# Kernel tuning notes

Measured on AMD Instinct MI355X. Metric: run time of the kernel, lower is better.

Reference implementation:

```python
import jax, jax.numpy as jnp
import numpy as np

N_USERS = 100000
N_MOVIES = 20000
E = 1000000
D_USER = 128
D_MOVIE = 404
HID = 256
OUT = 128


def setup_inputs() -> dict:
    key = jax.random.key(0)
    ks = jax.random.split(key, 20)
    s = 0.05
    inp = {
        'x_user': jax.random.normal(ks[0], (N_USERS, D_USER), jnp.float32),
        'x_movie': jax.random.normal(ks[1], (N_MOVIES, D_MOVIE), jnp.float32),
        'edge_src': jax.random.randint(ks[2], (E,), 0, N_USERS, jnp.int32),
        'edge_dst': jax.random.randint(ks[3], (E,), 0, N_MOVIES, jnp.int32),
        # layer 1, relation user-rates->movie: lin_l (on aggregated user msgs, with bias), lin_r (root, no bias)
        'w1_rm_l': jax.random.normal(ks[4], (D_USER, HID), jnp.float32) * s,
        'b1_rm': jnp.zeros((HID,), jnp.float32),
        'w1_rm_r': jax.random.normal(ks[5], (D_MOVIE, HID), jnp.float32) * s,
        # layer 1, relation movie-rev_rates->user
        'w1_mu_l': jax.random.normal(ks[6], (D_MOVIE, HID), jnp.float32) * s,
        'b1_mu': jnp.zeros((HID,), jnp.float32),
        'w1_mu_r': jax.random.normal(ks[7], (D_USER, HID), jnp.float32) * s,
        # layer 2, relation user-rates->movie
        'w2_rm_l': jax.random.normal(ks[8], (HID, OUT), jnp.float32) * s,
        'b2_rm': jnp.zeros((OUT,), jnp.float32),
        'w2_rm_r': jax.random.normal(ks[9], (HID, OUT), jnp.float32) * s,
        # layer 2, relation movie-rev_rates->user
        'w2_mu_l': jax.random.normal(ks[10], (HID, OUT), jnp.float32) * s,
        'b2_mu': jnp.zeros((OUT,), jnp.float32),
        'w2_mu_r': jax.random.normal(ks[11], (HID, OUT), jnp.float32) * s,
    }
    return inp


def _seg_mean(msgs, dst, n_dst):
    # mean-aggregate edge messages [E, d] into destination nodes [n_dst, d]
    s = jax.ops.segment_sum(msgs, dst, num_segments=n_dst)
    cnt = jax.ops.segment_sum(jnp.ones((dst.shape[0], 1), msgs.dtype), dst, num_segments=n_dst)
    return s / jnp.maximum(cnt, 1.0)


def _sage(x_src, x_dst, src, dst, n_dst, w_l, b_l, w_r):
    # PyG SAGEConv (mean aggr): lin_l(mean_{j->i} x_j) + lin_r(x_i)
    agg = _seg_mean(x_src[src], dst, n_dst)
    return agg @ w_l + b_l + x_dst @ w_r


def reference(x_user, x_movie, edge_src, edge_dst,
              w1_rm_l, b1_rm, w1_rm_r, w1_mu_l, b1_mu, w1_mu_r,
              w2_rm_l, b2_rm, w2_rm_r, w2_mu_l, b2_mu, w2_mu_r):
    # layer 1 (HeteroConv sum aggr is trivial: one relation per dst type) + relu
    h_movie = jax.nn.relu(_sage(x_user, x_movie, edge_src, edge_dst, N_MOVIES, w1_rm_l, b1_rm, w1_rm_r))
    h_user = jax.nn.relu(_sage(x_movie, x_user, edge_dst, edge_src, N_USERS, w1_mu_l, b1_mu, w1_mu_r))
    # layer 2 (no relu, matching the torch module)
    out_movie = _sage(h_user, h_movie, edge_src, edge_dst, N_MOVIES, w2_rm_l, b2_rm, w2_rm_r)
    out_user = _sage(h_movie, h_user, edge_dst, edge_src, N_USERS, w2_mu_l, b2_mu, w2_mu_r)
    return (out_movie, out_user)
```

## Files before the change

kernel.cpp:

```cpp
#include <hip/hip_runtime.h>
#include <cstddef>
#include <cstdint>

#define E_EDGES 1000000
#define NU 100000
#define NM 20000
#define DU 128
#define DM 404
#define HIDDIM 256
#define OUTDIM 128
#define XMW 544

typedef short bf8_t __attribute__((ext_vector_type(8)));
typedef float f32x4 __attribute__((ext_vector_type(4)));
typedef unsigned short u16x8 __attribute__((ext_vector_type(8)));

__device__ __forceinline__ float b2f(unsigned short u) {
  union { unsigned int i; float f; } x; x.i = ((unsigned int)u) << 16; return x.f;
}
__device__ __forceinline__ unsigned short f2b(float f) {
  union { float f; unsigned int i; } x; x.f = f;
  unsigned int r = x.i + 0x7FFFu + ((x.i >> 16) & 1u);
  return (unsigned short)(r >> 16);
}

#define GLOAD_LDS16(gp, lp)                                                      \
  __builtin_amdgcn_global_load_lds(                                              \
      (const __attribute__((address_space(1))) unsigned int*)(gp),               \
      (__attribute__((address_space(3))) unsigned int*)(lp), 16, 0, 0)

#define HISTB 977
__global__ __launch_bounds__(256) void hist_kernel(
    const int* __restrict__ esrc, const int* __restrict__ edst,
    int* __restrict__ deg_u, int* __restrict__ deg_m,
    int* __restrict__ rank_u, int* __restrict__ rank_m) {
  int e4 = blockIdx.x * 256 + threadIdx.x;
  if (e4 >= E_EDGES / 4) return;
  int4 s4 = reinterpret_cast<const int4*>(esrc)[e4];
  int4 d4 = reinterpret_cast<const int4*>(edst)[e4];
  int4 ru, rm;
  ru.x = atomicAdd(&deg_u[s4.x], 1);
  ru.y = atomicAdd(&deg_u[s4.y], 1);
  ru.z = atomicAdd(&deg_u[s4.z], 1);
  ru.w = atomicAdd(&deg_u[s4.w], 1);
  rm.x = atomicAdd(&deg_m[d4.x], 1);
  rm.y = atomicAdd(&deg_m[d4.y], 1);
  rm.z = atomicAdd(&deg_m[d4.z], 1);
  rm.w = atomicAdd(&deg_m[d4.w], 1);
  reinterpret_cast<int4*>(rank_u)[e4] = ru;
  reinterpret_cast<int4*>(rank_m)[e4] = rm;
}

__device__ __forceinline__ void scan_core_256(const int* __restrict__ deg,
                                              int* __restrict__ off, int n,
                                              int* wsum) {
  const int tid = threadIdx.x;
  const int lane = tid & 63;
  const int w = tid >> 6;
  int carry = 0;
  for (int base = 0; base < n; base += 4096) {
    const int i0 = base + tid * 16;
    int v[16];
    int s = 0;
    if (i0 + 16 <= n) {
#pragma unroll
      for (int q = 0; q < 4; ++q) {
        int4 t4 = *reinterpret_cast<const int4*>(&deg[i0 + q * 4]);
        v[q * 4 + 0] = t4.x; v[q * 4 + 1] = t4.y; v[q * 4 + 2] = t4.z; v[q * 4 + 3] = t4.w;
      }
    } else {
#pragma unroll
      for (int j = 0; j < 16; ++j) v[j] = (i0 + j < n) ? deg[i0 + j] : 0;
    }
#pragma unroll
    for (int j = 0; j < 16; ++j) s += v[j];
    int ws_ = s;
#pragma unroll
    for (int d = 1; d < 64; d <<= 1) {
      int t = __shfl_up(ws_, d, 64);
      if (lane >= d) ws_ += t;
    }
    if (lane == 63) wsum[w] = ws_;
    __syncthreads();
    int woff = 0, ctot = 0;
#pragma unroll
    for (int j = 0; j < 4; ++j) {
      int x = wsum[j];
      if (j < w) woff += x;
      ctot += x;
    }
    int ex = carry + woff + ws_ - s;
    if (i0 + 16 <= n) {
      int o[16];
#pragma unroll
      for (int j = 0; j < 16; ++j) { o[j] = ex; ex += v[j]; }
#pragma unroll
      for (int q = 0; q < 4; ++q)
        *reinterpret_cast<int4*>(&off[i0 + q * 4]) =
            make_int4(o[q * 4], o[q * 4 + 1], o[q * 4 + 2], o[q * 4 + 3]);
    } else {
#pragma unroll
      for (int j = 0; j < 16; ++j) {
        if (i0 + j < n) off[i0 + j] = ex;
        ex += v[j];
      }
    }
    carry += ctot;
    __syncthreads();
  }
  if (tid == 0) off[n] = carry;
}

#define PRA 3200000
#define PRB 5280000
#define PRC 5722368
__global__ __launch_bounds__(256) void scanprep_kernel(
    const int* __restrict__ deg_m, int* __restrict__ off_m,
    const int* __restrict__ deg_u, int* __restrict__ off_u,
    const float* __restrict__ x_user, unsigned short* __restrict__ xu_bf,
    const float* __restrict__ x_movie, unsigned short* __restrict__ xmcat,
    const float* __restrict__ w1_rm_l, const float* __restrict__ w1_rm_r,
    const float* __restrict__ w1_mu_l, const float* __restrict__ w1_mu_r,
    const float* __restrict__ w2_rm_l, const float* __restrict__ w2_mu_r,
    const float* __restrict__ w2_mu_l, const float* __restrict__ w2_rm_r,
    unsigned short* __restrict__ wL1, unsigned short* __restrict__ w1mur,
    unsigned short* __restrict__ wL2u, unsigned short* __restrict__ w2mul,
    unsigned short* __restrict__ w2rmr) {
  __shared__ int wsum[4];
  if (blockIdx.x == 0) { scan_core_256(deg_m, off_m, NM, wsum); return; }
  if (blockIdx.x == 1) { scan_core_256(deg_u, off_u, NU, wsum); return; }
  int j = (blockIdx.x - 2) * 256 + threadIdx.x;
  if (j < PRA) {
    float4 v = reinterpret_cast<const float4*>(x_user)[j];
    ushort4 o;
    o.x = f2b(v.x); o.y = f2b(v.y); o.z = f2b(v.z); o.w = f2b(v.w);
    reinterpret_cast<ushort4*>(xu_bf)[j] = o;
  } else if (j < PRB) {
    int q = j - PRA;
    int row = q / 104, c4 = (q % 104) * 4;
    ushort4 o;
    if (c4 < DM) {
      float4 v = *reinterpret_cast<const float4*>(&x_movie[(size_t)row * DM + c4]);
      o.x = f2b(v.x); o.y = f2b(v.y); o.z = f2b(v.z); o.w = f2b(v.w);
    } else {
      o.x = o.y = o.z = o.w = 0;
    }
    *reinterpret_cast<ushort4*>(&xmcat[(size_t)row * XMW + 128 + c4]) = o;
  } else if (j < PRC) {
    int q = j - PRB;
    if (q < 278528) {
      int n = q / 544, k = q % 544;
      float v = 0.f;
      if (n < 256) {
        if (k < 128) v = w1_rm_l[(size_t)k * 256 + n];
        else if (k < 532) v = w1_rm_r[(size_t)(k - 128) * 256 + n];
      } else {
        if (k >= 128 && k < 532) v = w1_mu_l[(size_t)(k - 128) * 256 + (n - 256)];
      }
      wL1[q] = f2b(v);
    } else if (q < 311296) {
      int p = q - 278528; int n = p / 128, k = p % 128;
      w1mur[p] = f2b(w1_mu_r[(size_t)k * 256 + n]);
    } else if (q < 376832) {
      int p = q - 311296; int n = p / 256, k = p % 256;
      float v = (n < 128) ? w2_rm_l[(size_t)k * 128 + n] : w2_mu_r[(size_t)k * 128 + (n - 128)];
      wL2u[p] = f2b(v);
    } else if (q < 409600) {
      int p = q - 376832; int n = p / 256, k = p % 256;
      w2mul[p] = f2b(w2_mu_l[(size_t)k * 128 + n]);
    } else {
      int p = q - 409600; int n = p / 256, k = p % 256;
      w2rmr[p] = f2b(w2_rm_r[(size_t)k * 128 + n]);
    }
  }
}

template <int MODE>
__device__ __forceinline__ void gemm_core(
    const unsigned short* __restrict__ A, int lda,
    const unsigned short* __restrict__ Bt, int ldb, int K,
    const unsigned short* __restrict__ elem, const float* __restrict__ bias,
    void* __restrict__ outA, int M, int bx, int by,
    unsigned short* Alds, unsigned short* Blds) {
  const int tid = threadIdx.x;
  const int w = tid >> 6, l = tid & 63;
  const int row0 = bx * 128;
  const int col0 = by * 128;
  const int wr = w >> 1, wc = w & 1;

  f32x4 acc[4][4] = {};

  int ar0 = row0 + w * 32 + (l >> 2);
  int ar1 = ar0 + 16;
  if (ar0 >= M) ar0 = M - 1;
  if (ar1 >= M) ar1 = M - 1;
  const size_t aoff0 = (size_t)ar0 * lda + (l & 3) * 8;
  const size_t aoff1 = (size_t)ar1 * lda + (l & 3) * 8;
  const int nr0 = col0 + w * 32 + (l >> 2);
  const size_t boff0 = (size_t)nr0 * ldb + (l & 3) * 8;
  const size_t boff1 = (size_t)(nr0 + 16) * ldb + (l & 3) * 8;
  unsigned short* aldsb = &Alds[w * 1024];
  unsigned short* bldsb = &Blds[w * 1024];

  for (int k0 = 0; k0 < K; k0 += 32) {
    GLOAD_LDS16(A + aoff0 + k0, aldsb);
    GLOAD_LDS16(A + aoff1 + k0, aldsb + 512);
    GLOAD_LDS16(Bt + boff0 + k0, bldsb);
    GLOAD_LDS16(Bt + boff1 + k0, bldsb + 512);
    __syncthreads();
    bf8_t af[4], bfr[4];
#pragma unroll
    for (int mi = 0; mi < 4; ++mi)
      af[mi] = *reinterpret_cast<const bf8_t*>(&Alds[(wr * 64 + mi * 16 + (l & 15)) * 32 + (l >> 4) * 8]);
#pragma unroll
    for (int nj = 0; nj < 4; ++nj)
      bfr[nj] = *reinterpret_cast<const bf8_t*>(&Blds[(wc * 64 + nj * 16 + (l & 15)) * 32 + (l >> 4) * 8]);
#pragma unroll
    for (int mi = 0; mi < 4; ++mi)
#pragma unroll
      for (int nj = 0; nj < 4; ++nj)
        acc[mi][nj] = __builtin_amdgcn_mfma_f32_16x16x32_bf16(af[mi], bfr[nj], acc[mi][nj], 0, 0, 0);
    __syncthreads();
  }

#pragma unroll
  for (int mi = 0; mi < 4; ++mi) {
    const int rbase = row0 + wr * 64 + mi * 16 + ((l >> 4) << 2);
#pragma unroll
    for (int nj = 0; nj < 4; ++nj) {
      const int col = col0 + wc * 64 + nj * 16 + (l & 15);
      float bb = 0.0f;
      if constexpr (MODE == 0 || MODE == 1 || MODE == 6) bb = bias[col];
#pragma unroll
      for (int r = 0; r < 4; ++r) {
        const int row = rbase + r;
        if (row >= M) continue;
        float v = acc[mi][nj][r] + bb;
        if constexpr (MODE == 1) v += b2f(elem[(size_t)row * 256 + col]);
        if constexpr (MODE == 0 || MODE == 1) v = fmaxf(v, 0.0f);
        if constexpr (MODE == 0 || MODE == 1 || MODE == 5) {
          ((unsigned short*)outA)[(size_t)row * 256 + col] = f2b(v);
        } else if constexpr (MODE == 2) {
          ((unsigned short*)outA)[(size_t)row * 128 + col] = f2b(v);
        } else {
          ((float*)outA)[(size_t)row * 128 + col] = v;
        }
      }
    }
  }
}

#define FILLB 977
__global__ __launch_bounds__(256) void fill_t1_kernel(
    const int* __restrict__ esrc, const int* __restrict__ edst,
    const int* __restrict__ rank_m, const int* __restrict__ rank_u,
    const int* __restrict__ off_m, const int* __restrict__ off_u,
    int* __restrict__ csr_m, int* __restrict__ csr_u,
    const unsigned short* __restrict__ A, const unsigned short* __restrict__ Bt,
    unsigned short* __restrict__ t1) {
  __shared__ unsigned short Alds[128 * 32];
  __shared__ unsigned short Blds[128 * 32];
  if (blockIdx.x < FILLB) {
    int e4 = blockIdx.x * 256 + threadIdx.x;
    if (e4 >= E_EDGES / 4) return;
    int4 s4 = reinterpret_cast<const int4*>(esrc)[e4];
    int4 d4 = reinterpret_cast<const int4*>(edst)[e4];
    int4 rm = reinterpret_cast<const int4*>(rank_m)[e4];
    int4 ru = reinterpret_cast<const int4*>(rank_u)[e4];
    csr_m[off_m[d4.x] + rm.x] = s4.x;
    csr_m[off_m[d4.y] + rm.y] = s4.y;
    csr_m[off_m[d4.z] + rm.z] = s4.z;
    csr_m[off_m[d4.w] + rm.w] = s4.w;
    csr_u[off_u[s4.x] + ru.x] = d4.x;
    csr_u[off_u[s4.y] + ru.y] = d4.y;
    csr_u[off_u[s4.z] + ru.z] = d4.z;
    csr_u[off_u[s4.w] + ru.w] = d4.w;
    return;
  }
  const int bi = blockIdx.x - FILLB;
  gemm_core<5>(A, XMW, Bt, XMW, 416, nullptr, nullptr, t1, NM,
               bi % 157, bi / 157, Alds, Blds);
}

template <int D>
__device__ __forceinline__ void gather_core(
    const unsigned short* __restrict__ table, const int* __restrict__ off,
    const int* __restrict__ idx, unsigned short* __restrict__ out,
    int n, int ostride, int bi) {
  constexpr int LPN = D / 8;
  constexpr int NPB = 256 / LPN;
  const int t = threadIdx.x;
  const int g = t / LPN;
  const int cl = (t % LPN) * 8;
  const int node = bi * NPB + g;
  if (node >= n) return;
  const int beg = off[node], end = off[node + 1];
  const float sc = 1.0f / fmaxf((float)(end - beg), 1.0f);
  float a[8] = {0, 0, 0, 0, 0, 0, 0, 0}, b[8] = {0, 0, 0, 0, 0, 0, 0, 0};
  int p = beg;
  for (; p + 3 < end; p += 4) {
    const int r0 = idx[p], r1 = idx[p + 1], r2 = idx[p + 2], r3 = idx[p + 3];
    u16x8 v0 = *reinterpret_cast<const u16x8*>(&table[(size_t)r0 * D + cl]);
    u16x8 v1 = *reinterpret_cast<const u16x8*>(&table[(size_t)r1 * D + cl]);
    u16x8 v2 = *reinterpret_cast<const u16x8*>(&table[(size_t)r2 * D + cl]);
    u16x8 v3 = *reinterpret_cast<const u16x8*>(&table[(size_t)r3 * D + cl]);
#pragma unroll
    for (int j = 0; j < 8; ++j) { a[j] += b2f(v0[j]); b[j] += b2f(v1[j]); }
#pragma unroll
    for (int j = 0; j < 8; ++j) { a[j] += b2f(v2[j]); b[j] += b2f(v3[j]); }
  }
  for (; p < end; ++p) {
    const int r0 = idx[p];
    u16x8 v0 = *reinterpret_cast<const u16x8*>(&table[(size_t)r0 * D + cl]);
#pragma unroll
    for (int j = 0; j < 8; ++j) a[j] += b2f(v0[j]);
  }
  u16x8 o;
#pragma unroll
  for (int j = 0; j < 8; ++j) o[j] = f2b((a[j] + b[j]) * sc);
  *reinterpret_cast<u16x8*>(&out[(size_t)node * ostride + cl]) = o;
}

__device__ __forceinline__ void gather_slice64(
    const unsigned short* __restrict__ table, int tstride,
    const int* __restrict__ off, const int* __restrict__ idx,
    unsigned short* __restrict__ out, int ostride, int n, int col0, int bi) {
  const int t = threadIdx.x;
  const int g = t >> 3;
  const int cl = col0 + (t & 7) * 8;
  const int node = bi * 32 + g;
  if (node >= n) return;
  const int beg = off[node], end = off[node + 1];
  const float sc = 1.0f / fmaxf((float)(end - beg), 1.0f);
  float a[8] = {0, 0, 0, 0, 0, 0, 0, 0}, b[8] = {0, 0, 0, 0, 0, 0, 0, 0};
  int p = beg;
  for (; p + 3 < end; p += 4) {
    const int r0 = idx[p], r1 = idx[p + 1], r2 = idx[p + 2], r3 = idx[p + 3];
    u16x8 v0 = *reinterpret_cast<const u16x8*>(&table[(size_t)r0 * tstride + cl]);
    u16x8 v1 = *reinterpret_cast<const u16x8*>(&table[(size_t)r1 * tstride + cl]);
    u16x8 v2 = *reinterpret_cast<const u16x8*>(&table[(size_t)r2 * tstride + cl]);
    u16x8 v3 = *reinterpret_cast<const u16x8*>(&table[(size_t)r3 * tstride + cl]);
#pragma unroll
    for (int j = 0; j < 8; ++j) { a[j] += b2f(v0[j]); b[j] += b2f(v1[j]); }
#pragma unroll
    for (int j = 0; j < 8; ++j) { a[j] += b2f(v2[j]); b[j] += b2f(v3[j]); }
  }
  for (; p < end; ++p) {
    const int r0 = idx[p];
    u16x8 v0 = *reinterpret_cast<const u16x8*>(&table[(size_t)r0 * tstride + cl]);
#pragma unroll
    for (int j = 0; j < 8; ++j) a[j] += b2f(v0[j]);
  }
  u16x8 o;
#pragma unroll
  for (int j = 0; j < 8; ++j) o[j] = f2b((a[j] + b[j]) * sc);
  *reinterpret_cast<u16x8*>(&out[(size_t)node * ostride + cl]) = o;
}

__device__ __forceinline__ void gather_add_slice64(
    const unsigned short* __restrict__ table, int tstride,
    const int* __restrict__ off, const int* __restrict__ idx,
    float* __restrict__ out, int ostride, int n, int col0, int bi) {
  const int t = threadIdx.x;
  const int g = t >> 3;
  const int cl = col0 + (t & 7) * 8;
  const int node = bi * 32 + g;
  if (node >= n) return;
  const int beg = off[node], end = off[node + 1];
  const float sc = 1.0f / fmaxf((float)(end - beg), 1.0f);
  float a[8] = {0, 0, 0, 0, 0, 0, 0, 0}, b[8] = {0, 0, 0, 0, 0, 0, 0, 0};
  int p = beg;
  for (; p + 3 < end; p += 4) {
    const int r0 = idx[p], r1 = idx[p + 1], r2 = idx[p + 2], r3 = idx[p + 3];
    u16x8 v0 = *reinterpret_cast<const u16x8*>(&table[(size_t)r0 * tstride + cl]);
    u16x8 v1 = *reinterpret_cast<const u16x8*>(&table[(size_t)r1 * tstride + cl]);
    u16x8 v2 = *reinterpret_cast<const u16x8*>(&table[(size_t)r2 * tstride + cl]);
    u16x8 v3 = *reinterpret_cast<const u16x8*>(&table[(size_t)r3 * tstride + cl]);
#pragma unroll
    for (int j = 0; j < 8; ++j) { a[j] += b2f(v0[j]); b[j] += b2f(v1[j]); }
#pragma unroll
    for (int j = 0; j < 8; ++j) { a[j] += b2f(v2[j]); b[j] += b2f(v3[j]); }
  }
  for (; p < end; ++p) {
    const int r0 = idx[p];
    u16x8 v0 = *reinterpret_cast<const u16x8*>(&table[(size_t)r0 * tstride + cl]);
#pragma unroll
    for (int j = 0; j < 8; ++j) a[j] += b2f(v0[j]);
  }
  float* dst = &out[(size_t)node * ostride + cl];
  float4 o0 = *reinterpret_cast<const float4*>(dst);
  float4 o1 = *reinterpret_cast<const float4*>(dst + 4);
  o0.x += (a[0] + b[0]) * sc; o0.y += (a[1] + b[1]) * sc;
  o0.z += (a[2] + b[2]) * sc; o0.w += (a[3] + b[3]) * sc;
  o1.x += (a[4] + b[4]) * sc; o1.y += (a[5] + b[5]) * sc;
  o1.z += (a[6] + b[6]) * sc; o1.w += (a[7] + b[7]) * sc;
  *reinterpret_cast<float4*>(dst) = o0;
  *reinterpret_cast<float4*>(dst + 4) = o1;
}

__device__ __forceinline__ void gather_add_f32_128(
    const unsigned short* __restrict__ table, const int* __restrict__ off,
    const int* __restrict__ idx, float* __restrict__ out, int n, int bi) {
  const int t = threadIdx.x;
  const int g = t >> 4;
  const int cl = (t & 15) * 8;
  const int node = bi * 16 + g;
  if (node >= n) return;
  const int beg = off[node], end = off[node + 1];
  const float sc = 1.0f / fmaxf((float)(end - beg), 1.0f);
  float a[8] = {0, 0, 0, 0, 0, 0, 0, 0}, b[8] = {0, 0, 0, 0, 0, 0, 0, 0};
  int p = beg;
  for (; p + 3 < end; p += 4) {
    const int r0 = idx[p], r1 = idx[p + 1], r2 = idx[p + 2], r3 = idx[p + 3];
    u16x8 v0 = *reinterpret_cast<const u16x8*>(&table[(size_t)r0 * 128 + cl]);
    u16x8 v1 = *reinterpret_cast<const u16x8*>(&table[(size_t)r1 * 128 + cl]);
    u16x8 v2 = *reinterpret_cast<const u16x8*>(&table[(size_t)r2 * 128 + cl]);
    u16x8 v3 = *reinterpret_cast<const u16x8*>(&table[(size_t)r3 * 128 + cl]);
#pragma unroll
    for (int j = 0; j < 8; ++j) { a[j] += b2f(v0[j]); b[j] += b2f(v1[j]); }
#pragma unroll
    for (int j = 0; j < 8; ++j) { a[j] += b2f(v2[j]); b[j] += b2f(v3[j]); }
  }
  for (; p < end; ++p) {
    const int r0 = idx[p];
    u16x8 v0 = *reinterpret_cast<const u16x8*>(&table[(size_t)r0 * 128 + cl]);
#pragma unroll
    for (int j = 0; j < 8; ++j) a[j] += b2f(v0[j]);
  }
  float* dst = &out[(size_t)node * 128 + cl];
  float4 o0 = *reinterpret_cast<const float4*>(dst);
  float4 o1 = *reinterpret_cast<const float4*>(dst + 4);
  o0.x += (a[0] + b[0]) * sc; o0.y += (a[1] + b[1]) * sc;
  o0.z += (a[2] + b[2]) * sc; o0.w += (a[3] + b[3]) * sc;
  o1.x += (a[4] + b[4]) * sc; o1.y += (a[5] + b[5]) * sc;
  o1.z += (a[6] + b[6]) * sc; o1.w += (a[7] + b[7]) * sc;
  *reinterpret_cast<float4*>(dst) = o0;
  *reinterpret_cast<float4*>(dst + 4) = o1;
}

__global__ __launch_bounds__(256) void gatherA_kernel(
    const unsigned short* __restrict__ t1, const int* __restrict__ off_u,
    const int* __restrict__ csr_u, unsigned short* __restrict__ M1u,
    const unsigned short* __restrict__ xu, const int* __restrict__ off_m,
    const int* __restrict__ csr_m, unsigned short* __restrict__ xmcat) {
  if (blockIdx.x < 12500) {
    const int s = blockIdx.x / 3125;
    const int bi = blockIdx.x % 3125;
    gather_slice64(t1, 256, off_u, csr_u, M1u, 256, NU, s * 64, bi);
  } else {
    gather_core<128>(xu, off_m, csr_m, xmcat, NM, XMW, blockIdx.x - 12500);
  }
}

__global__ __launch_bounds__(256) void gemmA_kernel(
    const unsigned short* __restrict__ xmcat, const unsigned short* __restrict__ wL1,
    const float* __restrict__ b1_rm, unsigned short* __restrict__ hm,
    const unsigned short* __restrict__ xu, const unsigned short* __restrict__ w1mur,
    const unsigned short* __restrict__ M1u, const float* __restrict__ b1_mu,
    unsigned short* __restrict__ hu) {
  __shared__ unsigned short Alds[128 * 32];
  __shared__ unsigned short Blds[128 * 32];
  if (blockIdx.x < 314) {
    int bi = blockIdx.x;
    gemm_core<0>(xmcat, XMW, wL1, XMW, XMW, nullptr, b1_rm, hm, NM,
                 bi % 157, bi / 157, Alds, Blds);
  } else {
    int bi = blockIdx.x - 314;
    gemm_core<1>(xu, 128, w1mur, 128, 128, M1u, b1_mu, hu, NU,
                 bi % 782, bi / 782, Alds, Blds);
  }
}

__global__ __launch_bounds__(256) void gemmB2_kernel(
    const unsigned short* __restrict__ hu, const unsigned short* __restrict__ w2rml,
    unsigned short* __restrict__ hul,
    const unsigned short* __restrict__ hm, const unsigned short* __restrict__ w2mul,
    unsigned short* __restrict__ t2,
    const unsigned short* __restrict__ w2mur, const float* __restrict__ b2_mu,
    float* __restrict__ out_user,
    const unsigned short* __restrict__ w2rmr, const float* __restrict__ b2_rm,
    float* __restrict__ out_movie) {
  __shared__ unsigned short Alds[128 * 32];
  __shared__ unsigned short Blds[128 * 32];
  if (blockIdx.x < 782) {
    gemm_core<2>(hu, 256, w2rml, 256, 256, nullptr, nullptr, hul, NU,
                 blockIdx.x, 0, Alds, Blds);
  } else if (blockIdx.x < 939) {
    gemm_core<2>(hm, 256, w2mul, 256, 256, nullptr, nullptr, t2, NM,
                 blockIdx.x - 782, 0, Alds, Blds);
  } else if (blockIdx.x < 1721) {
    gemm_core<6>(hu, 256, w2mur, 256, 256, nullptr, b2_mu, out_user, NU,
                 blockIdx.x - 939, 0, Alds, Blds);
  } else {
    gemm_core<6>(hm, 256, w2rmr, 256, 256, nullptr, b2_rm, out_movie, NM,
                 blockIdx.x - 1721, 0, Alds, Blds);
  }
}

__global__ __launch_bounds__(256) void gatherBC_kernel(
    const unsigned short* __restrict__ t2, const int* __restrict__ off_u,
    const int* __restrict__ csr_u, float* __restrict__ out_user,
    const unsigned short* __restrict__ hul, const int* __restrict__ off_m,
    const int* __restrict__ csr_m, float* __restrict__ out_movie) {
  if (blockIdx.x < 6250) {
    const int s = blockIdx.x / 3125;
    const int bi = blockIdx.x % 3125;
    gather_add_slice64(t2, 128, off_u, csr_u, out_user, 128, NU, s * 64, bi);
  } else {
    gather_add_f32_128(hul, off_m, csr_m, out_movie, NM, blockIdx.x - 6250);
  }
}

extern "C" void kernel_launch(void* const* d_in, const int* in_sizes, int n_in,
                              void* d_out, int out_size, void* d_ws, size_t ws_size,
                              hipStream_t stream) {
  const float* x_user  = (const float*)d_in[0];
  const float* x_movie = (const float*)d_in[1];
  const int*   esrc    = (const int*)d_in[2];
  const int*   edst    = (const int*)d_in[3];
  const float* w1_rm_l = (const float*)d_in[4];
  const float* b1_rm   = (const float*)d_in[5];
  const float* w1_rm_r = (const float*)d_in[6];
  const float* w1_mu_l = (const float*)d_in[7];
  const float* b1_mu   = (const float*)d_in[8];
  const float* w1_mu_r = (const float*)d_in[9];
  const float* w2_rm_l = (const float*)d_in[10];
  const float* b2_rm   = (const float*)d_in[11];
  const float* w2_rm_r = (const float*)d_in[12];
  const float* w2_mu_l = (const float*)d_in[13];
  const float* b2_mu   = (const float*)d_in[14];
  const float* w2_mu_r = (const float*)d_in[15];

  if (ws_size < 214240008ull) return;
  char* wsb = (char*)d_ws;
  unsigned short* xu_bf  = (unsigned short*)(wsb + 0);
  unsigned short* xmcat  = (unsigned short*)(wsb + 25600000);
  unsigned short* hm_bf  = (unsigned short*)(wsb + 47360000);
  unsigned short* t1_bf  = (unsigned short*)(wsb + 57600000);
  unsigned short* t2_bf  = (unsigned short*)(wsb + 67840000);
  unsigned short* M1u_bf = (unsigned short*)(wsb + 72960000);
  unsigned short* hul_bf = (unsigned short*)(wsb + 72960000);
  unsigned short* hu_bf  = (unsigned short*)(wsb + 149760000);
  int* rank_m = (int*)(wsb + 149760000);
  int* rank_u = (int*)(wsb + 153760000);
  unsigned short* wts = (unsigned short*)(wsb + 200960000);
  unsigned short* wL1_t   = wts;
  unsigned short* w1mur_t = wts + 278528;
  unsigned short* wL2u_t  = wts + 311296;
  unsigned short* w2mul_t = wts + 376832;
  unsigned short* w2rmr_t = wts + 409600;
  int* iw    = (int*)(wsb + 201844736);
  int* deg_m = iw;
  int* deg_u = iw + 20000;
  int* off_m = iw + 120000;
  int* off_u = iw + 140004;
  int* csr_m = iw + 240008;
  int* csr_u = iw + 1240008;

  float* out_movie = (float*)d_out;
  float* out_user  = (float*)d_out + (size_t)NM * OUTDIM;

  hipMemsetAsync(deg_m, 0, 120000 * sizeof(int), stream);
  hist_kernel<<<HISTB, 256, 0, stream>>>(esrc, edst, deg_u, deg_m, rank_u, rank_m);

  scanprep_kernel<<<2 + (PRC + 255) / 256, 256, 0, stream>>>(
      deg_m, off_m, deg_u, off_u,
      x_user, xu_bf, x_movie, xmcat,
      w1_rm_l, w1_rm_r, w1_mu_l, w1_mu_r, w2_rm_l, w2_mu_r, w2_mu_l, w2_rm_r,
      wL1_t, w1mur_t, wL2u_t, w2mul_t, w2rmr_t);

  fill_t1_kernel<<<FILLB + 314, 256, 0, stream>>>(
      esrc, edst, rank_m, rank_u, off_m, off_u, csr_m, csr_u,
      xmcat + 128, wL1_t + 256 * XMW + 128, t1_bf);

  gatherA_kernel<<<12500 + 1250, 256, 0, stream>>>(
      t1_bf, off_u, csr_u, M1u_bf, xu_bf, off_m, csr_m, xmcat);

  gemmA_kernel<<<314 + 1564, 256, 0, stream>>>(
      xmcat, wL1_t, b1_rm, hm_bf, xu_bf, w1mur_t, M1u_bf, b1_mu, hu_bf);

  gemmB2_kernel<<<1878, 256, 0, stream>>>(
      hu_bf, wL2u_t, hul_bf, hm_bf, w2mul_t, t2_bf,
      wL2u_t + 128 * 256, b2_mu, out_user, w2rmr_t, b2_rm, out_movie);

  gatherBC_kernel<<<6250 + 1250, 256, 0, stream>>>(
      t2_bf, off_u, csr_u, out_user, hul_bf, off_m, csr_m, out_movie);
}
```

Before: 448.9 us.

## Build CSR with two-level bucketed counting sort instead of global atomics

Replaces the global-atomic degree histogram, separate scan, and rank-based scatter with a radix-style two-pass bucket sort. Per-block LDS histograms over coarse buckets feed a small scan kernel. A second pass scatters packed edges into bucket buffers, and a third pass does per-bucket LDS counting to produce offsets and CSR. The aim is to remove contended global atomics and the memset, at the cost of an extra kernel launch and low-parallelism single-thread-per-bucket scan loops.

```diff
diff --git a/kernel.cpp b/kernel.cpp
--- a/kernel.cpp
+++ b/kernel.cpp
@@ -11,6 +11,11 @@
 #define OUTDIM 128
 #define XMW 544
 
+#define NBLK 64
+#define EPB 15625
+#define NBKT_M 313
+#define NBKT_U 196
+
 typedef short bf8_t __attribute__((ext_vector_type(8)));
 typedef float f32x4 __attribute__((ext_vector_type(4)));
 typedef unsigned short u16x8 __attribute__((ext_vector_type(8)));
@@ -29,94 +34,12 @@
       (const __attribute__((address_space(1))) unsigned int*)(gp),               \
       (__attribute__((address_space(3))) unsigned int*)(lp), 16, 0, 0)
 
-#define HISTB 977
-__global__ __launch_bounds__(256) void hist_kernel(
-    const int* __restrict__ esrc, const int* __restrict__ edst,
-    int* __restrict__ deg_u, int* __restrict__ deg_m,
-    int* __restrict__ rank_u, int* __restrict__ rank_m) {
-  int e4 = blockIdx.x * 256 + threadIdx.x;
-  if (e4 >= E_EDGES / 4) return;
-  int4 s4 = reinterpret_cast<const int4*>(esrc)[e4];
-  int4 d4 = reinterpret_cast<const int4*>(edst)[e4];
-  int4 ru, rm;
-  ru.x = atomicAdd(&deg_u[s4.x], 1);
-  ru.y = atomicAdd(&deg_u[s4.y], 1);
-  ru.z = atomicAdd(&deg_u[s4.z], 1);
-  ru.w = atomicAdd(&deg_u[s4.w], 1);
-  rm.x = atomicAdd(&deg_m[d4.x], 1);
-  rm.y = atomicAdd(&deg_m[d4.y], 1);
-  rm.z = atomicAdd(&deg_m[d4.z], 1);
-  rm.w = atomicAdd(&deg_m[d4.w], 1);
-  reinterpret_cast<int4*>(rank_u)[e4] = ru;
-  reinterpret_cast<int4*>(rank_m)[e4] = rm;
-}
-
-__device__ __forceinline__ void scan_core_256(const int* __restrict__ deg,
-                                              int* __restrict__ off, int n,
-                                              int* wsum) {
-  const int tid = threadIdx.x;
-  const int lane = tid & 63;
-  const int w = tid >> 6;
-  int carry = 0;
-  for (int base = 0; base < n; base += 4096) {
-    const int i0 = base + tid * 16;
-    int v[16];
-    int s = 0;
-    if (i0 + 16 <= n) {
-#pragma unroll
-      for (int q = 0; q < 4; ++q) {
-        int4 t4 = *reinterpret_cast<const int4*>(&deg[i0 + q * 4]);
-        v[q * 4 + 0] = t4.x; v[q * 4 + 1] = t4.y; v[q * 4 + 2] = t4.z; v[q * 4 + 3] = t4.w;
-      }
-    } else {
-#pragma unroll
-      for (int j = 0; j < 16; ++j) v[j] = (i0 + j < n) ? deg[i0 + j] : 0;
-    }
-#pragma unroll
-    for (int j = 0; j < 16; ++j) s += v[j];
-    int ws_ = s;
-#pragma unroll
-    for (int d = 1; d < 64; d <<= 1) {
-      int t = __shfl_up(ws_, d, 64);
-      if (lane >= d) ws_ += t;
-    }
-    if (lane == 63) wsum[w] = ws_;
-    __syncthreads();
-    int woff = 0, ctot = 0;
-#pragma unroll
-    for (int j = 0; j < 4; ++j) {
-      int x = wsum[j];
-      if (j < w) woff += x;
-      ctot += x;
-    }
-    int ex = carry + woff + ws_ - s;
-    if (i0 + 16 <= n) {
-      int o[16];
-#pragma unroll
-      for (int j = 0; j < 16; ++j) { o[j] = ex; ex += v[j]; }
-#pragma unroll
-      for (int q = 0; q < 4; ++q)
-        *reinterpret_cast<int4*>(&off[i0 + q * 4]) =
-            make_int4(o[q * 4], o[q * 4 + 1], o[q * 4 + 2], o[q * 4 + 3]);
-    } else {
-#pragma unroll
-      for (int j = 0; j < 16; ++j) {
-        if (i0 + j < n) off[i0 + j] = ex;
-        ex += v[j];
-      }
-    }
-    carry += ctot;
-    __syncthreads();
-  }
-  if (tid == 0) off[n] = carry;
-}
-
 #define PRA 3200000
 #define PRB 5280000
 #define PRC 5722368
-__global__ __launch_bounds__(256) void scanprep_kernel(
-    const int* __restrict__ deg_m, int* __restrict__ off_m,
-    const int* __restrict__ deg_u, int* __restrict__ off_u,
+__global__ __launch_bounds__(256) void passA_kernel(
+    const int* __restrict__ esrc, const int* __restrict__ edst,
+    int* __restrict__ cnt_m, int* __restrict__ cnt_u,
     const float* __restrict__ x_user, unsigned short* __restrict__ xu_bf,
     const float* __restrict__ x_movie, unsigned short* __restrict__ xmcat,
     const float* __restrict__ w1_rm_l, const float* __restrict__ w1_rm_r,
@@ -126,10 +49,32 @@
     unsigned short* __restrict__ wL1, unsigned short* __restrict__ w1mur,
     unsigned short* __restrict__ wL2u, unsigned short* __restrict__ w2mul,
     unsigned short* __restrict__ w2rmr) {
-  __shared__ int wsum[4];
-  if (blockIdx.x == 0) { scan_core_256(deg_m, off_m, NM, wsum); return; }
-  if (blockIdx.x == 1) { scan_core_256(deg_u, off_u, NU, wsum); return; }
-  int j = (blockIdx.x - 2) * 256 + threadIdx.x;
+  __shared__ int hist[NBKT_M];
+  const int bx = blockIdx.x;
+  if (bx < NBLK) {
+    for (int i = threadIdx.x; i < NBKT_M; i += 256) hist[i] = 0;
+    __syncthreads();
+    const int base = bx * EPB, end = base + EPB;
+    for (int i = base + threadIdx.x; i < end; i += 256)
+      atomicAdd(&hist[edst[i] >> 6], 1);
+    __syncthreads();
+    for (int i = threadIdx.x; i < NBKT_M; i += 256)
+      cnt_m[bx * NBKT_M + i] = hist[i];
+    return;
+  }
+  if (bx < 2 * NBLK) {
+    const int b = bx - NBLK;
+    for (int i = threadIdx.x; i < NBKT_U; i += 256) hist[i] = 0;
+    __syncthreads();
+    const int base = b * EPB, end = base + EPB;
+    for (int i = base + threadIdx.x; i < end; i += 256)
+      atomicAdd(&hist[esrc[i] >> 9], 1);
+    __syncthreads();
+    for (int i = threadIdx.x; i < NBKT_U; i += 256)
+      cnt_u[b * NBKT_U + i] = hist[i];
+    return;
+  }
+  int j = (bx - 2 * NBLK) * 256 + threadIdx.x;
   if (j < PRA) {
     float4 v = reinterpret_cast<const float4*>(x_user)[j];
     ushort4 o;
@@ -175,6 +120,47 @@
   }
 }
 
+__global__ __launch_bounds__(256) void scanAB_kernel(
+    int* __restrict__ cnt_m, int* __restrict__ base_m, int* __restrict__ bo_m,
+    int* __restrict__ cnt_u, int* __restrict__ base_u, int* __restrict__ bo_u) {
+  const int NB = blockIdx.x ? NBKT_U : NBKT_M;
+  const int* cnt = blockIdx.x ? cnt_u : cnt_m;
+  int* basep = blockIdx.x ? base_u : base_m;
+  int* bo = blockIdx.x ? bo_u : bo_m;
+  __shared__ int tot[NBKT_M];
+  for (int B = threadIdx.x; B < NB; B += 256) {
+    int s = 0;
+    for (int b = 0; b < NBLK; ++b) {
+      int c = cnt[b * NB + B];
+      basep[b * NB + B] = s;
+      s += c;
+    }
+    tot[B] = s;
+  }
+  __syncthreads();
+  if (threadIdx.x < 64) {
+    const int lane = threadIdx.x;
+    int carry = 0;
+    for (int c0 = 0; c0 < NB; c0 += 64) {
+      int v = (c0 + lane < NB) ? tot[c0 + lane] : 0;
+      int s = v;
+#pragma unroll
+      for (int d = 1; d < 64; d <<= 1) {
+        int t = __shfl_up(s, d, 64);
+        if (lane >= d) s += t;
+      }
+      if (c0 + lane < NB) bo[c0 + lane] = carry + s - v;
+      carry += __shfl(s, 63, 64);
+    }
+    if (lane == 0) bo[NB] = carry;
+  }
+  __syncthreads();
+  for (int B = threadIdx.x; B < NB; B += 256) {
+    const int b0 = bo[B];
+    for (int b = 0; b < NBLK; ++b) basep[b * NB + B] += b0;
+  }
+}
+
 template <int MODE>
 __device__ __forceinline__ void gemm_core(
     const unsigned short* __restrict__ A, int lda,
@@ -250,36 +236,115 @@
   }
 }
 
-#define FILLB 977
-__global__ __launch_bounds__(256) void fill_t1_kernel(
+__global__ __launch_bounds__(256) void passB_kernel(
     const int* __restrict__ esrc, const int* __restrict__ edst,
-    const int* __restrict__ rank_m, const int* __restrict__ rank_u,
-    const int* __restrict__ off_m, const int* __restrict__ off_u,
-    int* __restrict__ csr_m, int* __restrict__ csr_u,
+    const int* __restrict__ base_m, const int* __restrict__ base_u,
+    int* __restrict__ ebuf_m, int* __restrict__ ebuf_u,
     const unsigned short* __restrict__ A, const unsigned short* __restrict__ Bt,
     unsigned short* __restrict__ t1) {
   __shared__ unsigned short Alds[128 * 32];
   __shared__ unsigned short Blds[128 * 32];
-  if (blockIdx.x < FILLB) {
-    int e4 = blockIdx.x * 256 + threadIdx.x;
-    if (e4 >= E_EDGES / 4) return;
-    int4 s4 = reinterpret_cast<const int4*>(esrc)[e4];
-    int4 d4 = reinterpret_cast<const int4*>(edst)[e4];
-    int4 rm = reinterpret_cast<const int4*>(rank_m)[e4];
-    int4 ru = reinterpret_cast<const int4*>(rank_u)[e4];
-    csr_m[off_m[d4.x] + rm.x] = s4.x;
-    csr_m[off_m[d4.y] + rm.y] = s4.y;
-    csr_m[off_m[d4.z] + rm.z] = s4.z;
-    csr_m[off_m[d4.w] + rm.w] = s4.w;
-    csr_u[off_u[s4.x] + ru.x] = d4.x;
-    csr_u[off_u[s4.y] + ru.y] = d4.y;
-    csr_u[off_u[s4.z] + ru.z] = d4.z;
-    csr_u[off_u[s4.w] + ru.w] = d4.w;
+  const int bx = blockIdx.x;
+  if (bx < NBLK) {
+    int* cur = (int*)Alds;
+    for (int i = threadIdx.x; i < NBKT_M; i += 256) cur[i] = base_m[bx * NBKT_M + i];
+    __syncthreads();
+    const int base = bx * EPB, end = base + EPB;
+    for (int i = base + threadIdx.x; i < end; i += 256) {
+      const int d = edst[i], s = esrc[i];
+      const int pos = atomicAdd(&cur[d >> 6], 1);
+      ebuf_m[pos] = (s << 6) | (d & 63);
+    }
     return;
   }
-  const int bi = blockIdx.x - FILLB;
+  if (bx < 2 * NBLK) {
+    const int b = bx - NBLK;
+    int* cur = (int*)Alds;
+    for (int i = threadIdx.x; i < NBKT_U; i += 256) cur[i] = base_u[b * NBKT_U + i];
+    __syncthreads();
+    const int base = b * EPB, end = base + EPB;
+    for (int i = base + threadIdx.x; i < end; i += 256) {
+      const int d = edst[i], s = esrc[i];
+      const int pos = atomicAdd(&cur[s >> 9], 1);
+      ebuf_u[pos] = (d << 9) | (s & 511);
+    }
+    return;
+  }
+  const int bi = bx - 2 * NBLK;
   gemm_core<5>(A, XMW, Bt, XMW, 416, nullptr, nullptr, t1, NM,
                bi % 157, bi / 157, Alds, Blds);
+}
+
+__global__ __launch_bounds__(256) void passC_kernel(
+    const int* __restrict__ ebuf_m, const int* __restrict__ bo_m,
+    int* __restrict__ off_m, int* __restrict__ csr_m,
+    const int* __restrict__ ebuf_u, const int* __restrict__ bo_u,
+    int* __restrict__ off_u, int* __restrict__ csr_u) {
+  __shared__ int hist[512];
+  const int bx = blockIdx.x;
+  if (bx < NBKT_M) {
+    const int B = bx;
+    const int lo = bo_m[B], hi = bo_m[B + 1];
+    const int nbin = (NM - B * 64 < 64) ? (NM - B * 64) : 64;
+    for (int i = threadIdx.x; i < 64; i += 256) hist[i] = 0;
+    __syncthreads();
+    for (int i = lo + threadIdx.x; i < hi; i += 256)
+      atomicAdd(&hist[ebuf_m[i] & 63], 1);
+    __syncthreads();
+    if (threadIdx.x < 64) {
+      const int lane = threadIdx.x;
+      const int v = hist[lane];
+      int s = v;
+#pragma unroll
+      for (int d = 1; d < 64; d <<= 1) {
+        int t = __shfl_up(s, d, 64);
+        if (lane >= d) s += t;
+      }
+      const int ex = s - v;
+      if (lane < nbin) off_m[B * 64 + lane] = lo + ex;
+      if (B == NBKT_M - 1 && lane == 0) off_m[NM] = hi;
+      hist[lane] = ex;
+    }
+    __syncthreads();
+    for (int i = lo + threadIdx.x; i < hi; i += 256) {
+      const int p = ebuf_m[i];
+      const int pos = atomicAdd(&hist[p & 63], 1);
+      csr_m[lo + pos] = p >> 6;
+    }
+    return;
+  }
+  const int B = bx - NBKT_M;
+  const int lo = bo_u[B], hi = bo_u[B + 1];
+  const int nbin = (NU - B * 512 < 512) ? (NU - B * 512) : 512;
+  for (int i = threadIdx.x; i < 512; i += 256) hist[i] = 0;
+  __syncthreads();
+  for (int i = lo + threadIdx.x; i < hi; i += 256)
+    atomicAdd(&hist[ebuf_u[i] & 511], 1);
+  __syncthreads();
+  if (threadIdx.x < 64) {
+    const int lane = threadIdx.x;
+    int carry = 0;
+    for (int c0 = 0; c0 < 512; c0 += 64) {
+      const int v = hist[c0 + lane];
+      int s = v;
+#pragma unroll
+      for (int d = 1; d < 64; d <<= 1) {
+        int t = __shfl_up(s, d, 64);
+        if (lane >= d) s += t;
+      }
+      const int ex = carry + s - v;
+      if (c0 + lane < nbin) off_u[B * 512 + c0 + lane] = lo + ex;
+      hist[c0 + lane] = ex;
+      carry += __shfl(s, 63, 64);
+    }
+    if (B == NBKT_U - 1 && lane == 0) off_u[NU] = hi;
+  }
+  __syncthreads();
+  for (int i = lo + threadIdx.x; i < hi; i += 256) {
+    const int p = ebuf_u[i];
+    const int pos = atomicAdd(&hist[p & 511], 1);
+    csr_u[lo + pos] = p >> 9;
+  }
 }
 
 template <int D>
@@ -541,37 +606,43 @@
   unsigned short* M1u_bf = (unsigned short*)(wsb + 72960000);
   unsigned short* hul_bf = (unsigned short*)(wsb + 72960000);
   unsigned short* hu_bf  = (unsigned short*)(wsb + 149760000);
-  int* rank_m = (int*)(wsb + 149760000);
-  int* rank_u = (int*)(wsb + 153760000);
+  int* ebuf_m = (int*)(wsb + 149760000);
+  int* ebuf_u = (int*)(wsb + 153760000);
   unsigned short* wts = (unsigned short*)(wsb + 200960000);
   unsigned short* wL1_t   = wts;
   unsigned short* w1mur_t = wts + 278528;
   unsigned short* wL2u_t  = wts + 311296;
   unsigned short* w2mul_t = wts + 376832;
   unsigned short* w2rmr_t = wts + 409600;
-  int* iw    = (int*)(wsb + 201844736);
-  int* deg_m = iw;
-  int* deg_u = iw + 20000;
-  int* off_m = iw + 120000;
-  int* off_u = iw + 140004;
-  int* csr_m = iw + 240008;
-  int* csr_u = iw + 1240008;
+  int* iw     = (int*)(wsb + 201844736);
+  int* cnt_m  = iw;
+  int* base_m = iw + 20032;
+  int* cnt_u  = iw + 40064;
+  int* base_u = iw + 52608;
+  int* bo_m   = iw + 65152;
+  int* bo_u   = iw + 65466;
+  int* off_m  = iw + 120000;
+  int* off_u  = iw + 140004;
+  int* csr_m  = iw + 240008;
+  int* csr_u  = iw + 1240008;
 
   float* out_movie = (float*)d_out;
   float* out_user  = (float*)d_out + (size_t)NM * OUTDIM;
 
-  hipMemsetAsync(deg_m, 0, 120000 * sizeof(int), stream);
-  hist_kernel<<<HISTB, 256, 0, stream>>>(esrc, edst, deg_u, deg_m, rank_u, rank_m);
-
-  scanprep_kernel<<<2 + (PRC + 255) / 256, 256, 0, stream>>>(
-      deg_m, off_m, deg_u, off_u,
+  passA_kernel<<<2 * NBLK + (PRC + 255) / 256, 256, 0, stream>>>(
+      esrc, edst, cnt_m, cnt_u,
       x_user, xu_bf, x_movie, xmcat,
       w1_rm_l, w1_rm_r, w1_mu_l, w1_mu_r, w2_rm_l, w2_mu_r, w2_mu_l, w2_rm_r,
       wL1_t, w1mur_t, wL2u_t, w2mul_t, w2rmr_t);
 
-  fill_t1_kernel<<<FILLB + 314, 256, 0, stream>>>(
-      esrc, edst, rank_m, rank_u, off_m, off_u, csr_m, csr_u,
+  scanAB_kernel<<<2, 256, 0, stream>>>(cnt_m, base_m, bo_m, cnt_u, base_u, bo_u);
+
+  passB_kernel<<<2 * NBLK + 314, 256, 0, stream>>>(
+      esrc, edst, base_m, base_u, ebuf_m, ebuf_u,
       xmcat + 128, wL1_t + 256 * XMW + 128, t1_bf);
+
+  passC_kernel<<<NBKT_M + NBKT_U, 256, 0, stream>>>(
+      ebuf_m, bo_m, off_m, csr_m, ebuf_u, bo_u, off_u, csr_u);
 
   gatherA_kernel<<<12500 + 1250, 256, 0, stream>>>(
       t1_bf, off_u, csr_u, M1u_bf, xu_bf, off_m, csr_m, xmcat);
```

Measured after the change: 401.9 us (median of 3 runs). -10.5%, faster.
